# Optimization experiments

Hardware: AMD Instinct MI355X
Metric: run time of the kernel (lower is better)

The kernel has to match this reference:

```python
import jax, jax.numpy as jnp
import numpy as np

ATTN_MULT = 8.0
NEG_INF = float('-inf')

N, Q, S, D = 16, 2048, 2048, 64


def setup_inputs() -> dict:
    key = jax.random.key(0)
    kq, kk, kv, kp = jax.random.split(key, 4)
    return {
        "queries_nqd": jax.random.normal(kq, (N, Q, D), dtype=jnp.float32),
        "keys_nsd": jax.random.normal(kk, (N, S, D), dtype=jnp.float32),
        "values_nsv": jax.random.normal(kv, (N, S, D), dtype=jnp.float32),
        "prefix_len_n": jax.random.randint(kp, (N,), 0, S, dtype=jnp.int64 if jax.config.jax_enable_x64 else jnp.int32),
    }


def reference(queries_nqd, keys_nsd, values_nsv, prefix_len_n):
    # attention_type == 'block_diagonal', backend == 'torch', dropout p == 0
    n, q, d = queries_nqd.shape
    s = keys_nsd.shape[1]
    scale = ATTN_MULT / d
    # prefix-block mask: key position < prefix_len (broadcast over queries)
    block_mask_n1s = (jnp.arange(s)[None, None, :] < prefix_len_n[:, None, None])  # [n,1,s]
    diag_mask_qs = jnp.arange(q)[:, None] == jnp.arange(s)[None, :]                # [q,s]
    mask_nqs = block_mask_n1s | diag_mask_qs[None, :, :]                           # [n,q,s]
    scores_nqs = jnp.einsum('nqd,nsd->nqs', queries_nqd, keys_nsd) * scale
    scores_nqs = jnp.where(mask_nqs, scores_nqs, NEG_INF)
    probs_nqs = jax.nn.softmax(scores_nqs, axis=-1)
    return jnp.einsum('nqs,nsv->nqv', probs_nqs, values_nsv)
```

## Files before the change

kernel.cpp:

```cpp
#include <hip/hip_runtime.h>
#include <math.h>

#define NH 16
#define QL 2048
#define SL 2048
#define DD 64
#define PSTR 72
#define QK_SCALE_LOG2E 0.1803368801111f

typedef __attribute__((ext_vector_type(8))) short short8;
typedef __attribute__((ext_vector_type(4))) float floatx4;
typedef __attribute__((ext_vector_type(4))) unsigned short ushort4v;
typedef __attribute__((ext_vector_type(8))) unsigned short ushort8v;

__device__ __forceinline__ unsigned short f2bf(float x) {
    unsigned u = __float_as_uint(x);
    u += 0x7FFFu + ((u >> 16) & 1u);
    return (unsigned short)(u >> 16);
}

__device__ __forceinline__ void gld16(const unsigned short* g, unsigned short* l) {
    __builtin_amdgcn_global_load_lds(
        (const __attribute__((address_space(1))) unsigned int*)g,
        (__attribute__((address_space(3))) unsigned int*)l, 16, 0, 0);
}

__global__ __launch_bounds__(256) void prep(
    const float* __restrict__ Qf, const float* __restrict__ Kf, const float* __restrict__ Vf,
    unsigned short* __restrict__ Qb, unsigned short* __restrict__ Kb, unsigned short* __restrict__ Vtb)
{
    if (blockIdx.y < 2) {
        int idx = blockIdx.x * 256 + threadIdx.x;
        const float4* src; unsigned short* dst; float scale;
        if (blockIdx.y == 0) { src = (const float4*)Qf; dst = Qb; scale = QK_SCALE_LOG2E; }
        else                 { src = (const float4*)Kf; dst = Kb; scale = 1.0f; }
        float4 v = src[idx];
        ushort4v h = { f2bf(v.x * scale), f2bf(v.y * scale), f2bf(v.z * scale), f2bf(v.w * scale) };
        *(ushort4v*)(dst + (size_t)idx * 4) = h;
    } else {
        if (blockIdx.x >= 512) return;
        __shared__ unsigned short sT[64][PSTR];
        int bx = blockIdx.x;
        int n = bx >> 5, stile = bx & 31, s0 = stile * 64;
        int tid = (int)threadIdx.x;
        const float* vb = Vf + ((size_t)n * SL + s0) * DD;
        #pragma unroll
        for (int i = 0; i < 4; ++i) {
            int idx = tid + i * 256;
            int r = idx >> 4, c = (idx & 15) << 2;
            float4 v = *(const float4*)(vb + r * DD + c);
            sT[c + 0][r] = f2bf(v.x);
            sT[c + 1][r] = f2bf(v.y);
            sT[c + 2][r] = f2bf(v.z);
            sT[c + 3][r] = f2bf(v.w);
        }
        __syncthreads();
        int d = tid >> 2, sg = tid & 3;
        unsigned short* out = Vtb + (size_t)n * DD * SL + (size_t)d * SL + s0 + sg * 16;
        ushort8v a, b;
        #pragma unroll
        for (int i = 0; i < 8; ++i) { a[i] = sT[d][sg * 16 + i]; b[i] = sT[d][sg * 16 + 8 + i]; }
        *(ushort8v*)(out) = a;
        *(ushort8v*)(out + 8) = b;
    }
}

__global__ __launch_bounds__(256, 4) void attn_mfma_split(
    const unsigned short* __restrict__ Qb, const unsigned short* __restrict__ Kb,
    const unsigned short* __restrict__ Vtb, const int* __restrict__ plen_g,
    float* __restrict__ Op, float* __restrict__ Lp, int spl)
{
    __shared__ unsigned short sK[2][64 * 64];
    __shared__ unsigned short sVt[2][64 * 64];
    __shared__ unsigned short sP[4 * 16 * 64];

    const int blk = blockIdx.x;
    const int n  = blk & (NH - 1);
    const int qt = blk >> 4;
    const int q0 = qt * 64;
    const int sp = blockIdx.y;
    const int sbeg = sp * spl;
    const int plen = plen_g[n];
    const int ntile = spl >> 6;
    const bool hasdiag = (q0 >= sbeg) && (q0 < sbeg + spl);
    if (!((sbeg < plen) || hasdiag)) return;

    const int tid  = (int)threadIdx.x;
    const int wave = tid >> 6, lane = tid & 63, quad = lane >> 4, l16 = lane & 15;

    int rem  = plen - sbeg;
    int base = (rem > 0) ? min((rem + 63) >> 6, ntile) : 0;
    int td   = hasdiag ? ((q0 - sbeg) >> 6) : -1;
    int total = base + ((td >= base) ? 1 : 0);

    const int qrow  = wave * 16 + l16;
    const int qglob = q0 + qrow;
    const int pmask = (l16 & 7) * 8;

    const unsigned short* qg = Qb + ((size_t)(n * QL + qglob)) * DD + quad * 8;
    short8 bQ0 = *(const short8*)(qg);
    short8 bQ1 = *(const short8*)(qg + 32);

    const unsigned short* kh = Kb  + (size_t)n * SL * DD;
    const unsigned short* vh = Vtb + (size_t)n * DD * SL;

    const int seg0 = wave * 2, seg1 = wave * 2 + 1;
    const int r0 = seg0 * 8 + (lane >> 3), r1 = seg1 * 8 + (lane >> 3);
    const int cg0 = ((lane & 7) ^ (r0 & 7)) * 8, cg1 = ((lane & 7) ^ (r1 & 7)) * 8;

    {
        int t0 = (0 < base) ? 0 : td;
        const unsigned short* kg = kh + (size_t)(sbeg + t0 * 64) * DD;
        const unsigned short* vg = vh + (sbeg + t0 * 64);
        gld16(kg + r0 * DD + cg0, sK[0] + seg0 * 512);
        gld16(kg + r1 * DD + cg1, sK[0] + seg1 * 512);
        gld16(vg + (size_t)r0 * SL + cg0, sVt[0] + seg0 * 512);
        gld16(vg + (size_t)r1 * SL + cg1, sVt[0] + seg1 * 512);
    }

    floatx4 acc[4];
    #pragma unroll
    for (int dt = 0; dt < 4; ++dt) acc[dt] = (floatx4){0.f, 0.f, 0.f, 0.f};
    float lsum = 0.f;
    unsigned short* pw = sP + qrow * 64;

    for (int i = 0; i < total; ++i) {
        __syncthreads();

        if (i + 1 < total) {
            int tn = (i + 1 < base) ? (i + 1) : td;
            const unsigned short* kg = kh + (size_t)(sbeg + tn * 64) * DD;
            const unsigned short* vg = vh + (sbeg + tn * 64);
            unsigned short* dk = sK[(i + 1) & 1];
            unsigned short* dv = sVt[(i + 1) & 1];
            gld16(kg + r0 * DD + cg0, dk + seg0 * 512);
            gld16(kg + r1 * DD + cg1, dk + seg1 * 512);
            gld16(vg + (size_t)r0 * SL + cg0, dv + seg0 * 512);
            gld16(vg + (size_t)r1 * SL + cg1, dv + seg1 * 512);
        }

        const unsigned short* sk = sK[i & 1];
        const unsigned short* sv = sVt[i & 1];
        const int t  = (i < base) ? i : td;
        const int s0 = sbeg + t * 64;

        floatx4 sf[4];
        #pragma unroll
        for (int st2 = 0; st2 < 4; ++st2) sf[st2] = (floatx4){0.f, 0.f, 0.f, 0.f};
        #pragma unroll
        for (int st2 = 0; st2 < 4; ++st2) {
            int krow = st2 * 16 + l16;
            short8 aK0 = *(const short8*)(sk + krow * 64 + (((0 * 4 + quad) ^ (krow & 7)) * 8));
            short8 aK1 = *(const short8*)(sk + krow * 64 + (((1 * 4 + quad) ^ (krow & 7)) * 8));
            sf[st2] = __builtin_amdgcn_mfma_f32_16x16x32_bf16(aK0, bQ0, sf[st2], 0, 0, 0);
            sf[st2] = __builtin_amdgcn_mfma_f32_16x16x32_bf16(aK1, bQ1, sf[st2], 0, 0, 0);
        }

        if (s0 + 64 <= plen) {
            #pragma unroll
            for (int st2 = 0; st2 < 4; ++st2) {
                float p0 = __builtin_amdgcn_exp2f(sf[st2][0]);
                float p1 = __builtin_amdgcn_exp2f(sf[st2][1]);
                float p2 = __builtin_amdgcn_exp2f(sf[st2][2]);
                float p3 = __builtin_amdgcn_exp2f(sf[st2][3]);
                lsum += (p0 + p1) + (p2 + p3);
                ushort4v pk = { f2bf(p0), f2bf(p1), f2bf(p2), f2bf(p3) };
                *(ushort4v*)(pw + ((st2 * 16 + quad * 4) ^ pmask)) = pk;
            }
        } else {
            #pragma unroll
            for (int st2 = 0; st2 < 4; ++st2) {
                float p[4];
                #pragma unroll
                for (int r = 0; r < 4; ++r) {
                    int s = s0 + st2 * 16 + quad * 4 + r;
                    bool valid = (s < plen) || (s == qglob);
                    p[r] = __builtin_amdgcn_exp2f(valid ? sf[st2][r] : -INFINITY);
                    lsum += p[r];
                }
                ushort4v pk = { f2bf(p[0]), f2bf(p[1]), f2bf(p[2]), f2bf(p[3]) };
                *(ushort4v*)(pw + ((st2 * 16 + quad * 4) ^ pmask)) = pk;
            }
        }

        #pragma unroll
        for (int ks = 0; ks < 2; ++ks) {
            short8 aP = *(const short8*)(pw + ((ks * 32 + quad * 8) ^ pmask));
            #pragma unroll
            for (int dt = 0; dt < 4; ++dt) {
                int vrow = dt * 16 + l16;
                short8 bV = *(const short8*)(sv + vrow * 64 + (((ks * 4 + quad) ^ (vrow & 7)) * 8));
                acc[dt] = __builtin_amdgcn_mfma_f32_16x16x32_bf16(aP, bV, acc[dt], 0, 0, 0);
            }
        }
    }

    lsum += __shfl_xor(lsum, 16, 64);
    lsum += __shfl_xor(lsum, 32, 64);
    if (quad == 0)
        Lp[((size_t)sp * NH + n) * QL + q0 + qrow] = lsum;

    float* ob = Op + (((size_t)sp * NH + n) * QL + q0) * DD;
    #pragma unroll
    for (int r = 0; r < 4; ++r) {
        int ql = wave * 16 + quad * 4 + r;
        #pragma unroll
        for (int dt = 0; dt < 4; ++dt)
            ob[(size_t)ql * DD + dt * 16 + l16] = acc[dt][r];
    }
}

__global__ __launch_bounds__(256) void combine(
    const float* __restrict__ Op, const float* __restrict__ Lp,
    const int* __restrict__ plen_g, float* __restrict__ Og, int nsplit, int spl)
{
    int idx = blockIdx.x * 256 + (int)threadIdx.x;
    int d4 = idx & 15;
    int q  = (idx >> 4) & (QL - 1);
    int n  = idx >> 15;
    int plen = plen_g[n];
    int spd = q / spl;
    float4 s = {0.f, 0.f, 0.f, 0.f};
    float l = 0.f;
    for (int sp = 0; sp < nsplit; ++sp) {
        if ((sp * spl < plen) || (sp == spd)) {
            const float* ob = Op + (((size_t)sp * NH + n) * QL + q) * DD;
            float4 v = *(const float4*)(ob + d4 * 4);
            s.x += v.x; s.y += v.y; s.z += v.z; s.w += v.w;
            l += Lp[((size_t)sp * NH + n) * QL + q];
        }
    }
    float inv = 1.0f / l;
    float4 o = { s.x * inv, s.y * inv, s.z * inv, s.w * inv };
    *(float4*)(Og + ((size_t)n * QL + q) * DD + d4 * 4) = o;
}

extern "C" void kernel_launch(void* const* d_in, const int* in_sizes, int n_in,
                              void* d_out, int out_size, void* d_ws, size_t ws_size,
                              hipStream_t stream) {
    const float* Qf   = (const float*)d_in[0];
    const float* Kf   = (const float*)d_in[1];
    const float* Vf   = (const float*)d_in[2];
    const int*   plen = (const int*)d_in[3];
    float* Og = (float*)d_out;

    char* ws = (char*)d_ws;
    unsigned short* Qb  = (unsigned short*)(ws);
    unsigned short* Kb  = (unsigned short*)(ws + (4u << 20));
    unsigned short* Vtb = (unsigned short*)(ws + (8u << 20));
    float* Op = (float*)(ws + (12u << 20));

    const size_t op_bytes = (size_t)NH * QL * DD * 4;
    const size_t lp_bytes = (size_t)NH * QL * 4;
    int nsplit = 1;
    if (ws_size >= (12u << 20) + 4 * (op_bytes + lp_bytes)) nsplit = 4;
    else if (ws_size >= (12u << 20) + 2 * (op_bytes + lp_bytes)) nsplit = 2;
    float* Lp = (float*)(ws + (12u << 20) + (size_t)nsplit * op_bytes);
    int spl = SL / nsplit;

    prep<<<dim3(2048, 3), 256, 0, stream>>>(Qf, Kf, Vf, Qb, Kb, Vtb);
    attn_mfma_split<<<dim3(NH * (QL / 64), nsplit), 256, 0, stream>>>(Qb, Kb, Vtb, plen, Op, Lp, spl);
    combine<<<2048, 256, 0, stream>>>(Op, Lp, plen, Og, nsplit, spl);
}
```

Before: 111.8 us.

## Fuse Q conversion into attention and store split partials as bf16

Q is now loaded as fp32, scaled and converted to bf16 inside the attention kernel, so the prep pass no longer writes a bf16 Q copy. Split partial outputs are staged through LDS and written as bf16 with coalesced 16-byte stores, and combine reads them as bf16. Probabilities are packed with a paired bf16 conversion intrinsic. This cuts global memory traffic for Q and the partial outputs, at the cost of extra rounding error in the partials before they are combined.

Result: no change. 111.5 us (-0.3%).

```diff
diff --git a/kernel.cpp b/kernel.cpp
--- a/kernel.cpp
+++ b/kernel.cpp
@@ -1,4 +1,5 @@
 #include <hip/hip_runtime.h>
+#include <hip/hip_bf16.h>
 #include <math.h>
 
 #define NH 16
@@ -18,6 +19,13 @@
     u += 0x7FFFu + ((u >> 16) & 1u);
     return (unsigned short)(u >> 16);
 }
+__device__ __forceinline__ unsigned int f2bf2u(float x, float y) {
+    __hip_bfloat162 h = __float22bfloat162_rn(make_float2(x, y));
+    return *(unsigned int*)&h;
+}
+__device__ __forceinline__ float bf2f(unsigned short h) {
+    return __uint_as_float((unsigned)h << 16);
+}
 
 __device__ __forceinline__ void gld16(const unsigned short* g, unsigned short* l) {
     __builtin_amdgcn_global_load_lds(
@@ -26,17 +34,14 @@
 }
 
 __global__ __launch_bounds__(256) void prep(
-    const float* __restrict__ Qf, const float* __restrict__ Kf, const float* __restrict__ Vf,
-    unsigned short* __restrict__ Qb, unsigned short* __restrict__ Kb, unsigned short* __restrict__ Vtb)
+    const float* __restrict__ Kf, const float* __restrict__ Vf,
+    unsigned short* __restrict__ Kb, unsigned short* __restrict__ Vtb)
 {
-    if (blockIdx.y < 2) {
+    if (blockIdx.y == 0) {
         int idx = blockIdx.x * 256 + threadIdx.x;
-        const float4* src; unsigned short* dst; float scale;
-        if (blockIdx.y == 0) { src = (const float4*)Qf; dst = Qb; scale = QK_SCALE_LOG2E; }
-        else                 { src = (const float4*)Kf; dst = Kb; scale = 1.0f; }
-        float4 v = src[idx];
-        ushort4v h = { f2bf(v.x * scale), f2bf(v.y * scale), f2bf(v.z * scale), f2bf(v.w * scale) };
-        *(ushort4v*)(dst + (size_t)idx * 4) = h;
+        float4 v = ((const float4*)Kf)[idx];
+        ushort4v h = { f2bf(v.x), f2bf(v.y), f2bf(v.z), f2bf(v.w) };
+        *(ushort4v*)(Kb + (size_t)idx * 4) = h;
     } else {
         if (blockIdx.x >= 512) return;
         __shared__ unsigned short sT[64][PSTR];
@@ -66,9 +71,9 @@
 }
 
 __global__ __launch_bounds__(256, 4) void attn_mfma_split(
-    const unsigned short* __restrict__ Qb, const unsigned short* __restrict__ Kb,
+    const float* __restrict__ Qf, const unsigned short* __restrict__ Kb,
     const unsigned short* __restrict__ Vtb, const int* __restrict__ plen_g,
-    float* __restrict__ Op, float* __restrict__ Lp, int spl)
+    unsigned short* __restrict__ Opb, float* __restrict__ Lp, int spl)
 {
     __shared__ unsigned short sK[2][64 * 64];
     __shared__ unsigned short sVt[2][64 * 64];
@@ -97,9 +102,23 @@
     const int qglob = q0 + qrow;
     const int pmask = (l16 & 7) * 8;
 
-    const unsigned short* qg = Qb + ((size_t)(n * QL + qglob)) * DD + quad * 8;
-    short8 bQ0 = *(const short8*)(qg);
-    short8 bQ1 = *(const short8*)(qg + 32);
+    short8 bQ0, bQ1;
+    {
+        const float* qf = Qf + ((size_t)(n * QL + qglob)) * DD + quad * 8;
+        float4 a0 = *(const float4*)(qf);
+        float4 a1 = *(const float4*)(qf + 4);
+        float4 c0 = *(const float4*)(qf + 32);
+        float4 c1 = *(const float4*)(qf + 36);
+        const float S = QK_SCALE_LOG2E;
+        unsigned int u0[4] = {
+            f2bf2u(a0.x * S, a0.y * S), f2bf2u(a0.z * S, a0.w * S),
+            f2bf2u(a1.x * S, a1.y * S), f2bf2u(a1.z * S, a1.w * S) };
+        unsigned int u1[4] = {
+            f2bf2u(c0.x * S, c0.y * S), f2bf2u(c0.z * S, c0.w * S),
+            f2bf2u(c1.x * S, c1.y * S), f2bf2u(c1.z * S, c1.w * S) };
+        bQ0 = *(short8*)u0;
+        bQ1 = *(short8*)u1;
+    }
 
     const unsigned short* kh = Kb  + (size_t)n * SL * DD;
     const unsigned short* vh = Vtb + (size_t)n * DD * SL;
@@ -164,8 +183,8 @@
                 float p2 = __builtin_amdgcn_exp2f(sf[st2][2]);
                 float p3 = __builtin_amdgcn_exp2f(sf[st2][3]);
                 lsum += (p0 + p1) + (p2 + p3);
-                ushort4v pk = { f2bf(p0), f2bf(p1), f2bf(p2), f2bf(p3) };
-                *(ushort4v*)(pw + ((st2 * 16 + quad * 4) ^ pmask)) = pk;
+                uint2 pk = { f2bf2u(p0, p1), f2bf2u(p2, p3) };
+                *(uint2*)(pw + ((st2 * 16 + quad * 4) ^ pmask)) = pk;
             }
         } else {
             #pragma unroll
@@ -178,8 +197,8 @@
                     p[r] = __builtin_amdgcn_exp2f(valid ? sf[st2][r] : -INFINITY);
                     lsum += p[r];
                 }
-                ushort4v pk = { f2bf(p[0]), f2bf(p[1]), f2bf(p[2]), f2bf(p[3]) };
-                *(ushort4v*)(pw + ((st2 * 16 + quad * 4) ^ pmask)) = pk;
+                uint2 pk = { f2bf2u(p[0], p[1]), f2bf2u(p[2], p[3]) };
+                *(uint2*)(pw + ((st2 * 16 + quad * 4) ^ pmask)) = pk;
             }
         }
 
@@ -200,18 +219,30 @@
     if (quad == 0)
         Lp[((size_t)sp * NH + n) * QL + q0 + qrow] = lsum;
 
-    float* ob = Op + (((size_t)sp * NH + n) * QL + q0) * DD;
+    unsigned short* pws = sP + wave * 16 * 64;
     #pragma unroll
-    for (int r = 0; r < 4; ++r) {
-        int ql = wave * 16 + quad * 4 + r;
-        #pragma unroll
-        for (int dt = 0; dt < 4; ++dt)
-            ob[(size_t)ql * DD + dt * 16 + l16] = acc[dt][r];
+    for (int dt = 0; dt < 4; ++dt) {
+        int chunk = dt * 2 + (l16 >> 3);
+        #pragma unroll
+        for (int r = 0; r < 4; ++r) {
+            int row = quad * 4 + r;
+            int sw = ((chunk ^ (row & 7)) * 8) + (l16 & 7);
+            pws[row * 64 + sw] = f2bf(acc[dt][r]);
+        }
+    }
+    const size_t qbase = ((size_t)sp * NH + n) * QL + q0 + wave * 16;
+    #pragma unroll
+    for (int t = 0; t < 2; ++t) {
+        int row = t * 8 + (lane >> 3);
+        int chunk = lane & 7;
+        int sw = (chunk ^ (row & 7)) * 8;
+        ushort8v val = *(const ushort8v*)(pws + row * 64 + sw);
+        *(ushort8v*)(Opb + (qbase + row) * DD + chunk * 8) = val;
     }
 }
 
 __global__ __launch_bounds__(256) void combine(
-    const float* __restrict__ Op, const float* __restrict__ Lp,
+    const unsigned short* __restrict__ Opb, const float* __restrict__ Lp,
     const int* __restrict__ plen_g, float* __restrict__ Og, int nsplit, int spl)
 {
     int idx = blockIdx.x * 256 + (int)threadIdx.x;
@@ -224,9 +255,9 @@
     float l = 0.f;
     for (int sp = 0; sp < nsplit; ++sp) {
         if ((sp * spl < plen) || (sp == spd)) {
-            const float* ob = Op + (((size_t)sp * NH + n) * QL + q) * DD;
-            float4 v = *(const float4*)(ob + d4 * 4);
-            s.x += v.x; s.y += v.y; s.z += v.z; s.w += v.w;
+            const unsigned short* ob = Opb + (((size_t)sp * NH + n) * QL + q) * DD + d4 * 4;
+            ushort4v v = *(const ushort4v*)(ob);
+            s.x += bf2f(v[0]); s.y += bf2f(v[1]); s.z += bf2f(v[2]); s.w += bf2f(v[3]);
             l += Lp[((size_t)sp * NH + n) * QL + q];
         }
     }
@@ -245,20 +276,19 @@
     float* Og = (float*)d_out;
 
     char* ws = (char*)d_ws;
-    unsigned short* Qb  = (unsigned short*)(ws);
-    unsigned short* Kb  = (unsigned short*)(ws + (4u << 20));
-    unsigned short* Vtb = (unsigned short*)(ws + (8u << 20));
-    float* Op = (float*)(ws + (12u << 20));
-
-    const size_t op_bytes = (size_t)NH * QL * DD * 4;
+    unsigned short* Kb  = (unsigned short*)(ws);
+    unsigned short* Vtb = (unsigned short*)(ws + (4u << 20));
+    unsigned short* Opb = (unsigned short*)(ws + (8u << 20));
+
+    const size_t op_bytes = (size_t)NH * QL * DD * 2;
     const size_t lp_bytes = (size_t)NH * QL * 4;
     int nsplit = 1;
-    if (ws_size >= (12u << 20) + 4 * (op_bytes + lp_bytes)) nsplit = 4;
-    else if (ws_size >= (12u << 20) + 2 * (op_bytes + lp_bytes)) nsplit = 2;
-    float* Lp = (float*)(ws + (12u << 20) + (size_t)nsplit * op_bytes);
+    if (ws_size >= (8u << 20) + 4 * (op_bytes + lp_bytes)) nsplit = 4;
+    else if (ws_size >= (8u << 20) + 2 * (op_bytes + lp_bytes)) nsplit = 2;
+    float* Lp = (float*)(ws + (8u << 20) + (size_t)nsplit * op_bytes);
     int spl = SL / nsplit;
 
-    prep<<<dim3(2048, 3), 256, 0, stream>>>(Qf, Kf, Vf, Qb, Kb, Vtb);
-    attn_mfma_split<<<dim3(NH * (QL / 64), nsplit), 256, 0, stream>>>(Qb, Kb, Vtb, plen, Op, Lp, spl);
-    combine<<<2048, 256, 0, stream>>>(Op, Lp, plen, Og, nsplit, spl);
-}
+    prep<<<dim3(2048, 2), 256, 0, stream>>>(Kf, Vf, Kb, Vtb);
+    attn_mfma_split<<<dim3(NH * (QL / 64), nsplit), 256, 0, stream>>>(Qf, Kb, Vtb, plen, Opb, Lp, spl);
+    combine<<<2048, 256, 0, stream>>>(Opb, Lp, plen, Og, nsplit, spl);
+}
```
